# Kernel tuning notes

Measured on AMD Instinct MI355X. Metric: run time of the kernel, lower is better.

## Reference

```python
import jax, jax.numpy as jnp
import numpy as np

B, T_ENC, ENC_DIM = 32, 200, 256
T_DEC, DEC_OUT = 200, 80
HID = 256
PRENET1, PRENET2 = 256, 128


def _gru_cell(x, h, kernel, rec_kernel, bias):
    # Keras GRUCell, reset_after=True. bias: [2, 3*units] (input bias, recurrent bias)
    xz, xr, xh = jnp.split(x @ kernel + bias[0], 3, axis=-1)
    rz, rr, rh = jnp.split(h @ rec_kernel + bias[1], 3, axis=-1)
    z = jax.nn.sigmoid(xz + rz)
    r = jax.nn.sigmoid(xr + rr)
    hh = jnp.tanh(xh + r * rh)
    return z * h + (1.0 - z) * hh


def setup_inputs() -> dict:
    key = jax.random.key(0)
    ks = jax.random.split(key, 24)
    g = lambda k, shape: (jax.random.normal(k, shape, dtype=jnp.float32) / np.sqrt(shape[0] if len(shape) > 1 else 1.0))
    attn_in = PRENET2 + ENC_DIM  # prenet output concat prev attention
    return {
        "memory": jax.random.normal(ks[0], (B, T_ENC, ENC_DIM), dtype=jnp.float32),
        "dec_inputs": jax.random.normal(ks[1], (B, T_DEC, DEC_OUT), dtype=jnp.float32),
        # Prenet
        "fc1_w": g(ks[2], (DEC_OUT, PRENET1)), "fc1_b": jnp.zeros((PRENET1,), jnp.float32),
        "fc2_w": g(ks[3], (PRENET1, PRENET2)), "fc2_b": jnp.zeros((PRENET2,), jnp.float32),
        # Attention GRU cell
        "attn_k": g(ks[4], (attn_in, 3 * HID)), "attn_rk": g(ks[5], (HID, 3 * HID)),
        "attn_bias": jnp.zeros((2, 3 * HID), jnp.float32),
        # Bahdanau attention
        "W": g(ks[6], (ENC_DIM, ENC_DIM)), "U": g(ks[7], (HID, ENC_DIM)), "V": g(ks[8], (ENC_DIM, 1)),
        # Projection
        "proj_w": g(ks[9], (ENC_DIM + HID, HID)), "proj_b": jnp.zeros((HID,), jnp.float32),
        # Decoder GRU cells
        "rnn1_k": g(ks[10], (HID, 3 * HID)), "rnn1_rk": g(ks[11], (HID, 3 * HID)),
        "rnn1_bias": jnp.zeros((2, 3 * HID), jnp.float32),
        "rnn2_k": g(ks[12], (HID, 3 * HID)), "rnn2_rk": g(ks[13], (HID, 3 * HID)),
        "rnn2_bias": jnp.zeros((2, 3 * HID), jnp.float32),
        # Output projection
        "out_w": g(ks[14], (HID, DEC_OUT)), "out_b": jnp.zeros((DEC_OUT,), jnp.float32),
    }


def reference(memory, dec_inputs, fc1_w, fc1_b, fc2_w, fc2_b, attn_k, attn_rk,
              attn_bias, W, U, V, proj_w, proj_b, rnn1_k, rnn1_rk, rnn1_bias,
              rnn2_k, rnn2_rk, rnn2_bias, out_w, out_b):
    b = memory.shape[0]
    # W(values) is loop-invariant -> precompute (same math as in-step application)
    Wv = memory @ W  # [B, T_enc, ENC_DIM]

    def step(carry, x_t):
        attn, h_a, h1, h2 = carry
        # Prenet (Dropout is identity at inference)
        q = jax.nn.relu(x_t @ fc1_w + fc1_b)
        q = jax.nn.relu(q @ fc2_w + fc2_b)
        # Attention RNN
        h_a = _gru_cell(jnp.concatenate([q, attn], axis=-1), h_a, attn_k, attn_rk, attn_bias)
        # Bahdanau attention
        score = jnp.tanh(Wv + (h_a @ U)[:, None, :]) @ V           # [B, T_enc, 1]
        align = jax.nn.softmax(score, axis=1)                       # [B, T_enc, 1]
        attn = jnp.sum(align * memory, axis=1)                      # [B, ENC_DIM]
        # Projection + 2 decoder GRU cells with residual adds
        proj = jnp.concatenate([attn, h_a], axis=-1) @ proj_w + proj_b
        h1 = _gru_cell(proj, h1, rnn1_k, rnn1_rk, rnn1_bias)
        r1 = proj + h1
        h2 = _gru_cell(r1, h2, rnn2_k, rnn2_rk, rnn2_bias)
        r2 = r1 + h2
        out = r2 @ out_w + out_b
        return (attn, h_a, h1, h2), out

    init = (
        jnp.zeros((b, memory.shape[2]), memory.dtype),  # attention
        jnp.zeros((b, HID), memory.dtype),              # attn rnn state
        jnp.zeros((b, HID), memory.dtype),              # dec rnn1 state
        jnp.zeros((b, HID), memory.dtype),              # dec rnn2 state
    )
    xs = jnp.swapaxes(dec_inputs, 0, 1)  # [T_dec, B, DEC_OUT]
    _, ys = jax.lax.scan(step, init, xs)
    return jnp.swapaxes(ys, 0, 1)  # all_outputs: [B, T_dec, DEC_OUT]
```

## Files before the change

### kernel.cpp

```cpp
#include <hip/hip_runtime.h>
#include <math.h>


#define TENC 200
#define TDEC 200

typedef short bf16x8 __attribute__((ext_vector_type(8)));
typedef float f32x4  __attribute__((ext_vector_type(4)));

#define O_H1B 8192
#define O_H2B 24576
#define O_R1B 40960
#define O_AT  57344
#define O_NPQ 73728
#define O_ZPQ 98304
#define O_PJ  98432
#define ZERO_FLOATS 106624
#define O_HAS 106624
#define O_Q2  (O_HAS + 200*32*256)
#define O_WV  (O_Q2 + 200*32*128)
#define O_R2S (O_WV + 32*200*256)
#define O_IMG (O_R2S + 200*32*256)

#define IMGA_OFF  0u
#define IMGC1_OFF 1327104u
#define IMGC2_OFF 1859584u
#define IMGD_OFF  2924544u

__device__ __forceinline__ float sigm(float x)  { return 1.0f / (1.0f + __expf(-x)); }
__device__ __forceinline__ float ftanh(float x) { return 1.0f - 2.0f / (1.0f + __expf(2.0f * x)); }

__device__ __forceinline__ unsigned short f2bf(float f) {
  union { float f; unsigned u; } v; v.f = f;
  return (unsigned short)((v.u + 0x7FFFu + ((v.u >> 16) & 1u)) >> 16);
}
__device__ __forceinline__ float bf2f(unsigned short h) {
  union { unsigned u; float f; } v; v.u = ((unsigned)h) << 16; return v.f;
}

__device__ __forceinline__ void gst(float* p, float v) {
  __hip_atomic_store(p, v, __ATOMIC_RELAXED, __HIP_MEMORY_SCOPE_AGENT);
}
__device__ __forceinline__ float gld(const float* p) {
  return __hip_atomic_load(p, __ATOMIC_RELAXED, __HIP_MEMORY_SCOPE_AGENT);
}

__device__ __forceinline__ void pollwait(const unsigned* p, unsigned tgt, bool act) {
  for (;;) {
    bool ok = true;
    if (act) ok = (__hip_atomic_load(p, __ATOMIC_RELAXED, __HIP_MEMORY_SCOPE_AGENT) >= tgt);
    if (__syncthreads_and((int)ok)) break;
    __builtin_amdgcn_s_sleep(2);
  }
  asm volatile("" ::: "memory");
}
__device__ __forceinline__ void set_flag(unsigned* f, unsigned v) {
  asm volatile("" ::: "memory");
  __builtin_amdgcn_s_waitcnt(0);
  __syncthreads();
  if (threadIdx.x == 0) {
    __hip_atomic_store(f, v, __ATOMIC_RELAXED, __HIP_MEMORY_SCOPE_AGENT);
  }
}

__global__ __launch_bounds__(256) void k_prep(
    const float* __restrict__ aK, const float* __restrict__ aRK,
    const float* __restrict__ Wp,
    const float* __restrict__ K1, const float* __restrict__ RK1,
    const float* __restrict__ K2, const float* __restrict__ RK2,
    unsigned short* __restrict__ img)
{
  int e = blockIdx.x * 256 + threadIdx.x;
  int id = blockIdx.y;
  float w = 0.f; size_t oh = 0, ol = 0;
  if (id == 0) {
    if (e >= 32*32*648) return;
    int k = e % 648, n = (e / 648) & 31, blk = e / (648*32);
    int u = blk*8 + (n & 7), g = n >> 3;
    if (k < 384) {
      w = (g==0) ? aK[(size_t)k*768+u] : (g==1) ? aK[(size_t)k*768+256+u]
        : (g==2) ? aK[(size_t)k*768+512+u] : 0.f;
    } else if (k < 640) {
      int kk = k - 384;
      w = (g==0) ? aRK[(size_t)kk*768+u] : (g==1) ? aRK[(size_t)kk*768+256+u]
        : (g==3) ? aRK[(size_t)kk*768+512+u] : 0.f;
    }
    size_t base = IMGA_OFF + (size_t)blk*2*32*648;
    oh = base + (size_t)n*648 + k; ol = oh + 32*648;
  } else if (id == 1) {
    if (e >= 32*16*520) return;
    int k = e % 520, n = (e / 520) & 15, blk = e / (520*16);
    if (n < 8 && k < 512) w = Wp[(size_t)k*256 + blk*8 + n];
    size_t base = IMGC1_OFF + (size_t)blk*2*16*520;
    oh = base + (size_t)n*520 + k; ol = oh + 16*520;
  } else {
    if (e >= 32*32*520) return;
    int k = e % 520, n = (e / 520) & 31, blk = e / (520*32);
    int u = blk*8 + (n & 7), g = n >> 3;
    const float* Kx = (id == 2) ? K1 : K2;
    const float* Rx = (id == 2) ? RK1 : RK2;
    if (k < 256) {
      w = (g==0) ? Kx[(size_t)k*768+u] : (g==1) ? Kx[(size_t)k*768+256+u]
        : (g==2) ? Kx[(size_t)k*768+512+u] : 0.f;
    } else if (k < 512) {
      int kk = k - 256;
      w = (g==0) ? Rx[(size_t)kk*768+u] : (g==1) ? Rx[(size_t)kk*768+256+u]
        : (g==3) ? Rx[(size_t)kk*768+512+u] : 0.f;
    }
    size_t base = ((id == 2) ? IMGC2_OFF : IMGD_OFF) + (size_t)blk*2*32*520;
    oh = base + (size_t)n*520 + k; ol = oh + 32*520;
  }
  unsigned short hi = f2bf(w);
  unsigned short lo = f2bf(w - bf2f(hi));
  img[oh] = hi; img[ol] = lo;
}

__global__ __launch_bounds__(256, 1) void k_scan8(
    const float* __restrict__ memg,
    const float* __restrict__ aB, const float* __restrict__ Uw,
    const float* __restrict__ Vw, const float* __restrict__ pb,
    const float* __restrict__ B1v, const float* __restrict__ B2v,
    float* __restrict__ ws)
{
  const int tid = threadIdx.x, bid = blockIdx.x;
  const int lane = tid & 63, wv = tid >> 6;
  unsigned* fl = (unsigned*)ws;
  float* fH1B = ws + O_H1B;  float* fH2B = ws + O_H2B;  float* fR1B = ws + O_R1B;
  float* fAT  = ws + O_AT;   float* fNPq = ws + O_NPQ;  float* fZPq = ws + O_ZPQ;
  float* fPJ  = ws + O_PJ;   float* fHAS = ws + O_HAS;
  float* fQ2  = ws + O_Q2;   float* fWV  = ws + O_WV;   float* fR2S = ws + O_R2S;
  const unsigned short* img = (const unsigned short*)(ws + O_IMG);

  __shared__ __align__(16) char smem[140544];

  if (bid < 32) {
    const int j = bid;
    unsigned* myflag = fl + j * 32;
    unsigned short* sW = (unsigned short*)smem;
    unsigned short* sX = (unsigned short*)(smem + 82944);
    float* sOut = (float*)(smem + 124416);
    float* sHP  = (float*)(smem + 129024);
    float* sB   = (float*)(smem + 130048);
    {
      const uint4* src = (const uint4*)(img + IMGA_OFF + (size_t)j*2*32*648);
      uint4* dst = (uint4*)sW;
      for (int i = tid; i < 82944/16; i += 256) dst[i] = src[i];
      if (tid < 8) {
        int u = j*8 + tid;
        sB[tid]      = aB[u]       + aB[768 + u];
        sB[8 + tid]  = aB[256 + u] + aB[1024 + u];
        sB[16 + tid] = aB[512 + u];
        sB[24 + tid] = aB[1280 + u];
      }
    }
    __syncthreads();
    for (int t = 0; t < TDEC; ++t) {
      for (int i = tid; i < 4096; i += 256) {
        int b = i >> 7, k = i & 127;
        sX[b*648 + k] = f2bf(fQ2[((size_t)t*32 + b)*128 + k]);
      }
      pollwait(fl + (128 + (tid & 31))*32, (unsigned)t, (t > 0) && (tid < 32));
      float* at = fAT + (size_t)((t-1) & 1)*8192;
      for (int i = tid; i < 8192; i += 256) {
        int b = i >> 8, d = i & 255;
        float v = (t > 0) ? gld(at + b*256 + d) : 0.f;
        sX[b*648 + 128 + d] = f2bf(v);
      }
      for (int i = tid; i < 8192; i += 256) {
        int b = i >> 8, d = i & 255;
        float v = (t > 0) ? gld(fHAS + ((size_t)(t-1)*32 + b)*256 + d) : 0.f;
        sX[b*648 + 384 + d] = f2bf(v);
      }
      { int b = tid >> 3, ul = tid & 7;
        sHP[tid] = (t > 0) ? gld(fHAS + ((size_t)(t-1)*32 + b)*256 + j*8 + ul) : 0.f; }
      __syncthreads();
      {
        const int mt = wv >> 1, nt = wv & 1;
        f32x4 acc = {0.f, 0.f, 0.f, 0.f};
        const unsigned short* xr = sX + (size_t)(mt*16 + (lane&15))*648 + ((lane>>4)*8);
        const unsigned short* wh = sW + (size_t)(nt*16 + (lane&15))*648 + ((lane>>4)*8);
        const unsigned short* wl = wh + 32*648;
        for (int kt = 0; kt < 20; ++kt) {
          bf16x8 a  = *(const bf16x8*)(xr + kt*32);
          bf16x8 bh = *(const bf16x8*)(wh + kt*32);
          bf16x8 bl = *(const bf16x8*)(wl + kt*32);
          acc = __builtin_amdgcn_mfma_f32_16x16x32_bf16(a, bh, acc, 0, 0, 0);
          acc = __builtin_amdgcn_mfma_f32_16x16x32_bf16(a, bl, acc, 0, 0, 0);
        }
        int r0 = mt*16 + ((lane>>4)<<2), c = nt*16 + (lane&15);
        #pragma unroll
        for (int i2 = 0; i2 < 4; ++i2) sOut[(r0+i2)*36 + c] = acc[i2];
      }
      __syncthreads();
      { int b = tid >> 3, ul = tid & 7;
        float z = sigm(sOut[b*36 + ul] + sB[ul]);
        float r = sigm(sOut[b*36 + 8 + ul] + sB[8+ul]);
        float hh = ftanh(sOut[b*36 + 16 + ul] + sB[16+ul] + r*(sOut[b*36 + 24 + ul] + sB[24+ul]));
        float hn = z * sHP[tid] + (1.0f - z) * hh;
        gst(fHAS + ((size_t)t*32 + b)*256 + j*8 + ul, hn);
      }
      set_flag(myflag, (unsigned)(t + 1));
    }
  } else if (bid < 160) {
    const int idx = bid - 32, b = idx >> 2, q = idx & 3;
    unsigned* myflag = fl + (32 + b*3 + (q - 1)) * 32;
    float* sWV  = (float*)smem;
    float* sMem = (float*)(smem + 52000);
    float* sV   = (float*)(smem + 104000);
    float* sHA  = (float*)(smem + 105024);
    float* sUh  = (float*)(smem + 106048);
    float* sE   = (float*)(smem + 107072);
    float* sZ   = (float*)(smem + 107328);
    float* sCtx = (float*)(smem + 107392);
    float* sZs  = (float*)(smem + 108416);
    for (int i = tid; i < 50*256; i += 256) {
      int r = i >> 8, d = i & 255;
      sWV[r*260 + d]  = fWV[((size_t)b*200 + q*50 + r)*256 + d];
      sMem[r*260 + d] = memg[((size_t)b*200 + q*50 + r)*256 + d];
    }
    sV[tid] = Vw[tid];
    __syncthreads();
    for (int t = 0; t < TDEC; ++t) {
      pollwait(fl + (tid & 31)*32, (unsigned)(t + 1), tid < 32);
      sHA[tid] = gld(fHAS + ((size_t)t*32 + b)*256 + tid);
      __syncthreads();
      {
        float acc = 0.f;
        #pragma unroll 8
        for (int k = 0; k < 256; ++k) acc += sHA[k] * Uw[(size_t)k*256 + tid];
        sUh[tid] = acc; }
      __syncthreads();
      { int r = tid >> 2, qd = tid & 3;
        float part = 0.f;
        if (r < 50) {
          const float* wvp = sWV + r*260 + qd*64;
          const float* uh = sUh + qd*64;
          const float* vv = sV + qd*64;
          #pragma unroll 8
          for (int i2 = 0; i2 < 64; ++i2) part += vv[i2] * ftanh(wvp[i2] + uh[i2]);
        }
        part += __shfl_down(part, 2, 4);
        part += __shfl_down(part, 1, 4);
        if (r < 50 && qd == 0) sE[r] = __expf(part);
      }
      __syncthreads();
      if (tid < 64) {
        float e = (tid < 50) ? sE[tid] : 0.f;
        #pragma unroll
        for (int off = 32; off; off >>= 1) e += __shfl_xor(e, off, 64);
        if (tid == 0) sZ[0] = e;
      }
      __syncthreads();
      { float acc = 0.f;
        #pragma unroll 2
        for (int r = 0; r < 50; ++r) acc += sE[r] * sMem[r*260 + tid];
        if (q) gst(fNPq + ((size_t)b*3 + q - 1)*256 + tid, acc);
        else   sCtx[tid] = acc; }
      if (q) {
        if (tid == 0) gst(fZPq + b*3 + q - 1, sZ[0]);
        set_flag(myflag, (unsigned)(t + 1));
      } else {
        { const unsigned* p; unsigned tg; bool act;
          if (tid < 3)                    { p = fl + (32 + b*3 + tid)*32; tg = (unsigned)(t+1); act = true; }
          else if (tid >= 32 && tid < 64) { p = fl + (160 + tid - 32)*32; tg = (unsigned)(t-1); act = (t >= 2); }
          else                            { p = fl;                       tg = 0u;              act = false; }
          pollwait(p, tg, act);
        }
        if (tid < 3) sZs[tid] = gld(fZPq + b*3 + tid);
        __syncthreads();
        float Zi = 1.0f / (sZ[0] + sZs[0] + sZs[1] + sZs[2]);
        float av = (sCtx[tid] + gld(fNPq + (size_t)(b*3 + 0)*256 + tid)
                             + gld(fNPq + (size_t)(b*3 + 1)*256 + tid)
                             + gld(fNPq + (size_t)(b*3 + 2)*256 + tid)) * Zi;
        gst(fAT + (size_t)(t & 1)*8192 + b*256 + tid, av);
        set_flag(fl + (128 + b)*32, (unsigned)(t + 1));
      }
    }
  } else if (bid < 192) {
    const int j = bid - 160;
    unsigned* flagC1 = fl + (160 + j) * 32;
    unsigned* flagC2 = fl + (192 + j) * 32;
    unsigned short* sW1 = (unsigned short*)smem;
    unsigned short* sW2 = (unsigned short*)(smem + 33280);
    unsigned short* sX  = (unsigned short*)(smem + 99840);
    float* sOut = (float*)(smem + 133120);
    float* sPJ  = (float*)(smem + 137728);
    float* sH1p = (float*)(smem + 138752);
    float* sB   = (float*)(smem + 139776);
    {
      const uint4* s1 = (const uint4*)(img + IMGC1_OFF + (size_t)j*2*16*520);
      uint4* d1 = (uint4*)sW1;
      for (int i = tid; i < 33280/16; i += 256) d1[i] = s1[i];
      const uint4* s2 = (const uint4*)(img + IMGC2_OFF + (size_t)j*2*32*520);
      uint4* d2 = (uint4*)sW2;
      for (int i = tid; i < 66560/16; i += 256) d2[i] = s2[i];
      if (tid < 8) {
        int u = j*8 + tid;
        sB[tid]      = B1v[u]       + B1v[768 + u];
        sB[8 + tid]  = B1v[256 + u] + B1v[1024 + u];
        sB[16 + tid] = B1v[512 + u];
        sB[24 + tid] = B1v[1280 + u];
        sB[32 + tid] = pb[u];
      }
    }
    __syncthreads();
    for (int t = 0; t < TDEC; ++t) {
      {
        const unsigned* p; unsigned tg; bool act;
        if (tid < 32)      { p = fl + (128 + tid)*32;       tg = (unsigned)(t+1); act = true; }
        else if (tid < 64) { p = fl + (192 + tid - 32)*32;  tg = (unsigned)t;     act = (t > 0); }
        else if (tid < 96) { p = fl + (224 + tid - 64)*32;  tg = (unsigned)(t-1); act = (t >= 2); }
        else               { p = fl;                        tg = 0u;              act = false; }
        pollwait(p, tg, act);
      }
      float* at = fAT + (size_t)(t & 1)*8192;
      for (int i = tid; i < 8192; i += 256) {
        int b = i >> 8, d = i & 255;
        sX[b*520 + d] = f2bf(gld(at + b*256 + d));
      }
      for (int i = tid; i < 8192; i += 256) {
        int b = i >> 8, d = i & 255;
        sX[b*520 + 256 + d] = f2bf(gld(fHAS + ((size_t)t*32 + b)*256 + d));
      }
      __syncthreads();
      if (wv < 2) {
        const int mt = wv;
        f32x4 acc = {0.f, 0.f, 0.f, 0.f};
        const unsigned short* xr = sX + (size_t)(mt*16 + (lane&15))*520 + ((lane>>4)*8);
        const unsigned short* wh = sW1 + (size_t)(lane&15)*520 + ((lane>>4)*8);
        const unsigned short* wl = wh + 16*520;
        for (int kt = 0; kt < 16; ++kt) {
          bf16x8 a  = *(const bf16x8*)(xr + kt*32);
          bf16x8 bh = *(const bf16x8*)(wh + kt*32);
          bf16x8 bl = *(const bf16x8*)(wl + kt*32);
          acc = __builtin_amdgcn_mfma_f32_16x16x32_bf16(a, bh, acc, 0, 0, 0);
          acc = __builtin_amdgcn_mfma_f32_16x16x32_bf16(a, bl, acc, 0, 0, 0);
        }
        int r0 = mt*16 + ((lane>>4)<<2), c = lane & 15;
        #pragma unroll
        for (int i2 = 0; i2 < 4; ++i2) sOut[(r0+i2)*36 + c] = acc[i2];
      }
      __syncthreads();
      { int b = tid >> 3, ul = tid & 7;
        float pj = sOut[b*36 + ul] + sB[32 + ul];
        sPJ[tid] = pj;
        gst(fPJ + (size_t)b*256 + j*8 + ul, pj); }
      set_flag(flagC1, (unsigned)(t + 1));
      pollwait(fl + (160 + (tid & 31))*32, (unsigned)(t + 1), tid < 32);
      for (int i = tid; i < 8192; i += 256) {
        int b = i >> 8, d = i & 255;
        sX[b*520 + d] = f2bf(gld(fPJ + (size_t)b*256 + d));
      }
      for (int i = tid; i < 8192; i += 256) {
        int b = i >> 8, d = i & 255;
        sX[b*520 + 256 + d] = f2bf(gld(fH1B + (size_t)(t & 1)*8192 + (size_t)b*256 + d));
      }
      { int b = tid >> 3, ul = tid & 7;
        sH1p[tid] = gld(fH1B + (size_t)(t & 1)*8192 + (size_t)b*256 + j*8 + ul); }
      __syncthreads();
      {
        const int mt = wv >> 1, nt = wv & 1;
        f32x4 acc = {0.f, 0.f, 0.f, 0.f};
        const unsigned short* xr = sX + (size_t)(mt*16 + (lane&15))*520 + ((lane>>4)*8);
        const unsigned short* wh = sW2 + (size_t)(nt*16 + (lane&15))*520 + ((lane>>4)*8);
        const unsigned short* wl = wh + 32*520;
        for (int kt = 0; kt < 16; ++kt) {
          bf16x8 a  = *(const bf16x8*)(xr + kt*32);
          bf16x8 bh = *(const bf16x8*)(wh + kt*32);
          bf16x8 bl = *(const bf16x8*)(wl + kt*32);
          acc = __builtin_amdgcn_mfma_f32_16x16x32_bf16(a, bh, acc, 0, 0, 0);
          acc = __builtin_amdgcn_mfma_f32_16x16x32_bf16(a, bl, acc, 0, 0, 0);
        }
        int r0 = mt*16 + ((lane>>4)<<2), c = nt*16 + (lane&15);
        #pragma unroll
        for (int i2 = 0; i2 < 4; ++i2) sOut[(r0+i2)*36 + c] = acc[i2];
      }
      __syncthreads();
      { int b = tid >> 3, ul = tid & 7;
        float z = sigm(sOut[b*36 + ul] + sB[ul]);
        float r = sigm(sOut[b*36 + 8 + ul] + sB[8+ul]);
        float hh = ftanh(sOut[b*36 + 16 + ul] + sB[16+ul] + r*(sOut[b*36 + 24 + ul] + sB[24+ul]));
        float hn = z * sH1p[tid] + (1.0f - z) * hh;
        gst(fH1B + (size_t)((t+1) & 1)*8192 + (size_t)b*256 + j*8 + ul, hn);
        gst(fR1B + (size_t)(t & 1)*8192 + (size_t)b*256 + j*8 + ul, sPJ[tid] + hn);
      }
      set_flag(flagC2, (unsigned)(t + 1));
    }
  } else {
    const int j = bid - 192;
    unsigned* myflag = fl + (224 + j) * 32;
    unsigned short* sW = (unsigned short*)smem;
    unsigned short* sX = (unsigned short*)(smem + 66560);
    float* sOut = (float*)(smem + 99840);
    float* sR1f = (float*)(smem + 104448);
    float* sH2p = (float*)(smem + 105472);
    float* sB   = (float*)(smem + 106496);
    {
      const uint4* s2 = (const uint4*)(img + IMGD_OFF + (size_t)j*2*32*520);
      uint4* d2 = (uint4*)sW;
      for (int i = tid; i < 66560/16; i += 256) d2[i] = s2[i];
      if (tid < 8) {
        int u = j*8 + tid;
        sB[tid]      = B2v[u]       + B2v[768 + u];
        sB[8 + tid]  = B2v[256 + u] + B2v[1024 + u];
        sB[16 + tid] = B2v[512 + u];
        sB[24 + tid] = B2v[1280 + u];
      }
    }
    __syncthreads();
    for (int t = 0; t < TDEC; ++t) {
      { const unsigned* p; unsigned tg; bool act;
        if (tid < 32)      { p = fl + (192 + tid)*32;       tg = (unsigned)(t+1); act = true; }
        else if (tid < 64) { p = fl + (224 + tid - 32)*32;  tg = (unsigned)t;     act = (t > 0); }
        else               { p = fl;                        tg = 0u;              act = false; }
        pollwait(p, tg, act);
      }
      for (int i = tid; i < 8192; i += 256) {
        int b = i >> 8, d = i & 255;
        sX[b*520 + d] = f2bf(gld(fR1B + (size_t)(t & 1)*8192 + (size_t)b*256 + d));
      }
      for (int i = tid; i < 8192; i += 256) {
        int b = i >> 8, d = i & 255;
        sX[b*520 + 256 + d] = f2bf(gld(fH2B + (size_t)(t & 1)*8192 + (size_t)b*256 + d));
      }
      { int b = tid >> 3, ul = tid & 7;
        sR1f[tid] = gld(fR1B + (size_t)(t & 1)*8192 + (size_t)b*256 + j*8 + ul);
        sH2p[tid] = gld(fH2B + (size_t)(t & 1)*8192 + (size_t)b*256 + j*8 + ul); }
      __syncthreads();
      { const int mt = wv >> 1, nt = wv & 1;
        f32x4 acc = {0.f, 0.f, 0.f, 0.f};
        const unsigned short* xr = sX + (size_t)(mt*16 + (lane&15))*520 + ((lane>>4)*8);
        const unsigned short* wh = sW + (size_t)(nt*16 + (lane&15))*520 + ((lane>>4)*8);
        const unsigned short* wl = wh + 32*520;
        for (int kt = 0; kt < 16; ++kt) {
          bf16x8 a  = *(const bf16x8*)(xr + kt*32);
          bf16x8 bh = *(const bf16x8*)(wh + kt*32);
          bf16x8 bl = *(const bf16x8*)(wl + kt*32);
          acc = __builtin_amdgcn_mfma_f32_16x16x32_bf16(a, bh, acc, 0, 0, 0);
          acc = __builtin_amdgcn_mfma_f32_16x16x32_bf16(a, bl, acc, 0, 0, 0);
        }
        int r0 = mt*16 + ((lane>>4)<<2), c = nt*16 + (lane&15);
        #pragma unroll
        for (int i2 = 0; i2 < 4; ++i2) sOut[(r0+i2)*36 + c] = acc[i2];
      }
      __syncthreads();
      { int b = tid >> 3, ul = tid & 7;
        float z = sigm(sOut[b*36 + ul] + sB[ul]);
        float r = sigm(sOut[b*36 + 8 + ul] + sB[8+ul]);
        float hh = ftanh(sOut[b*36 + 16 + ul] + sB[16+ul] + r*(sOut[b*36 + 24 + ul] + sB[24+ul]));
        float hn = z * sH2p[tid] + (1.0f - z) * hh;
        gst(fH2B + (size_t)((t+1) & 1)*8192 + (size_t)b*256 + j*8 + ul, hn);
        fR2S[((size_t)t*32 + b)*256 + j*8 + ul] = sR1f[tid] + hn;
      }
      set_flag(myflag, (unsigned)(t + 1));
    }
  }
}

__global__ __launch_bounds__(256) void k_wv(
    const float* __restrict__ mem, const float* __restrict__ W, float* __restrict__ wv)
{
  const int tile = blockIdx.x, b = blockIdx.y;
  const int t0 = tile * 8, tid = threadIdx.x;
  __shared__ float rows[2048];
  for (int i = tid; i < 2048; i += 256) rows[i] = mem[((size_t)b*TENC + t0)*256 + i];
  __syncthreads();
  float acc[8] = {0,0,0,0,0,0,0,0};
  for (int k = 0; k < 256; ++k) {
    float w = W[(size_t)k*256 + tid];
    #pragma unroll
    for (int tt = 0; tt < 8; ++tt) acc[tt] += rows[tt*256 + k] * w;
  }
  #pragma unroll
  for (int tt = 0; tt < 8; ++tt) wv[((size_t)b*TENC + t0 + tt)*256 + tid] = acc[tt];
}

__global__ __launch_bounds__(256) void k_prenet(
    const float* __restrict__ x, const float* __restrict__ w1, const float* __restrict__ b1,
    const float* __restrict__ w2, const float* __restrict__ b2, float* __restrict__ q2)
{
  const int tile = blockIdx.x, b = blockIdx.y;
  const int t0 = tile * 4, tid = threadIdx.x;
  __shared__ float xr[320];
  __shared__ float q1[1024];
  for (int i = tid; i < 320; i += 256) {
    int tt = i / 80, k = i - tt*80;
    xr[i] = x[((size_t)b*TDEC + t0 + tt)*80 + k];
  }
  __syncthreads();
  {
    float a0 = 0.f, a1 = 0.f, a2 = 0.f, a3 = 0.f;
    for (int k = 0; k < 80; ++k) {
      float w = w1[(size_t)k*256 + tid];
      a0 += xr[k]*w; a1 += xr[80+k]*w; a2 += xr[160+k]*w; a3 += xr[240+k]*w;
    }
    float bb = b1[tid];
    q1[tid]       = fmaxf(a0 + bb, 0.f);
    q1[256 + tid] = fmaxf(a1 + bb, 0.f);
    q1[512 + tid] = fmaxf(a2 + bb, 0.f);
    q1[768 + tid] = fmaxf(a3 + bb, 0.f);
  }
  __syncthreads();
  {
    const int jj = tid & 127, tp = tid >> 7;
    float c0 = 0.f, c1 = 0.f;
    for (int k = 0; k < 256; ++k) {
      float w = w2[(size_t)k*128 + jj];
      c0 += q1[(2*tp)*256 + k] * w;
      c1 += q1[(2*tp + 1)*256 + k] * w;
    }
    float bb = b2[jj];
    q2[(((size_t)t0 + 2*tp)*32 + b)*128 + jj]     = fmaxf(c0 + bb, 0.f);
    q2[(((size_t)t0 + 2*tp + 1)*32 + b)*128 + jj] = fmaxf(c1 + bb, 0.f);
  }
}

__global__ __launch_bounds__(128) void k_out(
    const float* __restrict__ r2, const float* __restrict__ wo,
    const float* __restrict__ bo, float* __restrict__ out)
{
  const int tb = blockIdx.x;
  const int t = tb >> 5, b = tb & 31, tid = threadIdx.x;
  __shared__ float row[256];
  for (int i = tid; i < 256; i += 128) row[i] = r2[(size_t)tb*256 + i];
  __syncthreads();
  if (tid < 80) {
    float acc = bo[tid];
    #pragma unroll 4
    for (int k = 0; k < 256; ++k) acc += row[k] * wo[(size_t)k*80 + tid];
    out[((size_t)b*TDEC + t)*80 + tid] = acc;
  }
}

extern "C" void kernel_launch(void* const* d_in, const int* in_sizes, int n_in,
                              void* d_out, int out_size, void* d_ws, size_t ws_size,
                              hipStream_t stream)
{
  const float* mem = (const float*)d_in[0];
  const float* dec = (const float*)d_in[1];
  const float* w1  = (const float*)d_in[2];
  const float* b1  = (const float*)d_in[3];
  const float* w2  = (const float*)d_in[4];
  const float* b2  = (const float*)d_in[5];
  const float* aK  = (const float*)d_in[6];
  const float* aRK = (const float*)d_in[7];
  const float* aB  = (const float*)d_in[8];
  const float* W   = (const float*)d_in[9];
  const float* U   = (const float*)d_in[10];
  const float* V   = (const float*)d_in[11];
  const float* Wp  = (const float*)d_in[12];
  const float* pb  = (const float*)d_in[13];
  const float* K1  = (const float*)d_in[14];
  const float* RK1 = (const float*)d_in[15];
  const float* B1v = (const float*)d_in[16];
  const float* K2  = (const float*)d_in[17];
  const float* RK2 = (const float*)d_in[18];
  const float* B2v = (const float*)d_in[19];
  const float* Wo  = (const float*)d_in[20];
  const float* bo  = (const float*)d_in[21];
  float* ws  = (float*)d_ws;
  float* out = (float*)d_out;

  hipMemsetAsync(ws, 0, (size_t)ZERO_FLOATS * sizeof(float), stream);
  k_prep<<<dim3(2592, 4), 256, 0, stream>>>(aK, aRK, Wp, K1, RK1, K2, RK2,
                                            (unsigned short*)(ws + O_IMG));
  k_wv<<<dim3(25, 32), 256, 0, stream>>>(mem, W, ws + O_WV);
  k_prenet<<<dim3(50, 32), 256, 0, stream>>>(dec, w1, b1, w2, b2, ws + O_Q2);
  k_scan8<<<224, 256, 0, stream>>>(mem, aB, U, V, pb, B1v, B2v, ws);
  k_out<<<6400, 128, 0, stream>>>(ws + O_R2S, Wo, bo, out);
}
```

Baseline: 6.461 ms.

## Merge split-attention blocks into one block per batch and vectorize flag-guarded exchanges

Each batch's attention now runs in a single block instead of four blocks that exchanged partial context sums and normalizers through global memory. This removes one cross-block flag hop and the merge step in every decoder step, and the persistent grid shrinks from 224 to 128 blocks. To fit in shared memory, W·memory is stored in bf16 and memory rows are streamed from global each step. U is also pre-converted to bf16, and state exchanges use 64-bit atomic loads and stores plus shared-memory carry of the previous hidden state. The costs are lower precision in the attention scores, more serial work per attention block on the critical path, and heavier per-step global memory reads.

```diff
diff --git a/kernel.cpp b/kernel.cpp
--- a/kernel.cpp
+++ b/kernel.cpp
@@ -7,16 +7,16 @@
 
 typedef short bf16x8 __attribute__((ext_vector_type(8)));
 typedef float f32x4  __attribute__((ext_vector_type(4)));
+typedef float f32x2  __attribute__((ext_vector_type(2)));
+typedef unsigned short u16x2 __attribute__((ext_vector_type(2)));
 
 #define O_H1B 8192
 #define O_H2B 24576
 #define O_R1B 40960
 #define O_AT  57344
-#define O_NPQ 73728
-#define O_ZPQ 98304
-#define O_PJ  98432
-#define ZERO_FLOATS 106624
-#define O_HAS 106624
+#define O_PJ  73728
+#define ZERO_FLOATS 81920
+#define O_HAS 81920
 #define O_Q2  (O_HAS + 200*32*256)
 #define O_WV  (O_Q2 + 200*32*128)
 #define O_R2S (O_WV + 32*200*256)
@@ -26,6 +26,7 @@
 #define IMGC1_OFF 1327104u
 #define IMGC2_OFF 1859584u
 #define IMGD_OFF  2924544u
+#define IMGU_OFF  3989504u
 
 __device__ __forceinline__ float sigm(float x)  { return 1.0f / (1.0f + __expf(-x)); }
 __device__ __forceinline__ float ftanh(float x) { return 1.0f - 2.0f / (1.0f + __expf(2.0f * x)); }
@@ -38,11 +39,15 @@
   union { unsigned u; float f; } v; v.u = ((unsigned)h) << 16; return v.f;
 }
 
-__device__ __forceinline__ void gst(float* p, float v) {
-  __hip_atomic_store(p, v, __ATOMIC_RELAXED, __HIP_MEMORY_SCOPE_AGENT);
-}
-__device__ __forceinline__ float gld(const float* p) {
-  return __hip_atomic_load(p, __ATOMIC_RELAXED, __HIP_MEMORY_SCOPE_AGENT);
+__device__ __forceinline__ f32x2 gld2(const float* p) {
+  unsigned long long u = __hip_atomic_load((const unsigned long long*)p,
+                          __ATOMIC_RELAXED, __HIP_MEMORY_SCOPE_AGENT);
+  union { unsigned long long u; f32x2 f; } c; c.u = u; return c.f;
+}
+__device__ __forceinline__ void gst2(float* p, float a, float b) {
+  union { unsigned long long u; float f[2]; } c; c.f[0] = a; c.f[1] = b;
+  __hip_atomic_store((unsigned long long*)p, c.u,
+                     __ATOMIC_RELAXED, __HIP_MEMORY_SCOPE_AGENT);
 }
 
 __device__ __forceinline__ void pollwait(const unsigned* p, unsigned tgt, bool act) {
@@ -68,11 +73,16 @@
     const float* __restrict__ Wp,
     const float* __restrict__ K1, const float* __restrict__ RK1,
     const float* __restrict__ K2, const float* __restrict__ RK2,
+    const float* __restrict__ Uw,
     unsigned short* __restrict__ img)
 {
   int e = blockIdx.x * 256 + threadIdx.x;
   int id = blockIdx.y;
   float w = 0.f; size_t oh = 0, ol = 0;
+  if (id == 4) {
+    if (e < 256*256) img[IMGU_OFF + e] = f2bf(Uw[e]);
+    return;
+  }
   if (id == 0) {
     if (e >= 32*32*648) return;
     int k = e % 648, n = (e / 648) & 31, blk = e / (648*32);
@@ -115,10 +125,10 @@
   img[oh] = hi; img[ol] = lo;
 }
 
-__global__ __launch_bounds__(256, 1) void k_scan8(
+__global__ __launch_bounds__(256, 1) void k_scan9(
     const float* __restrict__ memg,
-    const float* __restrict__ aB, const float* __restrict__ Uw,
-    const float* __restrict__ Vw, const float* __restrict__ pb,
+    const float* __restrict__ aB, const float* __restrict__ Vw,
+    const float* __restrict__ pb,
     const float* __restrict__ B1v, const float* __restrict__ B2v,
     float* __restrict__ ws)
 {
@@ -126,8 +136,7 @@
   const int lane = tid & 63, wv = tid >> 6;
   unsigned* fl = (unsigned*)ws;
   float* fH1B = ws + O_H1B;  float* fH2B = ws + O_H2B;  float* fR1B = ws + O_R1B;
-  float* fAT  = ws + O_AT;   float* fNPq = ws + O_NPQ;  float* fZPq = ws + O_ZPQ;
-  float* fPJ  = ws + O_PJ;   float* fHAS = ws + O_HAS;
+  float* fAT  = ws + O_AT;   float* fPJ  = ws + O_PJ;   float* fHAS = ws + O_HAS;
   float* fQ2  = ws + O_Q2;   float* fWV  = ws + O_WV;   float* fR2S = ws + O_R2S;
   const unsigned short* img = (const unsigned short*)(ws + O_IMG);
 
@@ -139,7 +148,7 @@
     unsigned short* sW = (unsigned short*)smem;
     unsigned short* sX = (unsigned short*)(smem + 82944);
     float* sOut = (float*)(smem + 124416);
-    float* sHP  = (float*)(smem + 129024);
+    float* sHNp = (float*)(smem + 129024);
     float* sB   = (float*)(smem + 130048);
     {
       const uint4* src = (const uint4*)(img + IMGA_OFF + (size_t)j*2*32*648);
@@ -152,27 +161,29 @@
         sB[16 + tid] = aB[512 + u];
         sB[24 + tid] = aB[1280 + u];
       }
+      sHNp[tid & 255] = 0.f;
     }
     __syncthreads();
     for (int t = 0; t < TDEC; ++t) {
-      for (int i = tid; i < 4096; i += 256) {
-        int b = i >> 7, k = i & 127;
-        sX[b*648 + k] = f2bf(fQ2[((size_t)t*32 + b)*128 + k]);
-      }
-      pollwait(fl + (128 + (tid & 31))*32, (unsigned)t, (t > 0) && (tid < 32));
+      for (int i = tid; i < 2048; i += 256) {
+        int b = i >> 6, dp = i & 63;
+        f32x2 v = *(const f32x2*)(fQ2 + ((size_t)t*32 + b)*128 + dp*2);
+        *(u16x2*)(sX + b*648 + dp*2) = (u16x2){f2bf(v.x), f2bf(v.y)};
+      }
+      pollwait(fl + (32 + (tid & 31))*32, (unsigned)t, (t > 0) && (tid < 32));
       float* at = fAT + (size_t)((t-1) & 1)*8192;
-      for (int i = tid; i < 8192; i += 256) {
-        int b = i >> 8, d = i & 255;
-        float v = (t > 0) ? gld(at + b*256 + d) : 0.f;
-        sX[b*648 + 128 + d] = f2bf(v);
-      }
-      for (int i = tid; i < 8192; i += 256) {
-        int b = i >> 8, d = i & 255;
-        float v = (t > 0) ? gld(fHAS + ((size_t)(t-1)*32 + b)*256 + d) : 0.f;
-        sX[b*648 + 384 + d] = f2bf(v);
-      }
-      { int b = tid >> 3, ul = tid & 7;
-        sHP[tid] = (t > 0) ? gld(fHAS + ((size_t)(t-1)*32 + b)*256 + j*8 + ul) : 0.f; }
+      for (int i = tid; i < 4096; i += 256) {
+        int b = i >> 7, dp = i & 127;
+        f32x2 v; if (t > 0) v = gld2(at + b*256 + dp*2); else { v.x = 0.f; v.y = 0.f; }
+        *(u16x2*)(sX + b*648 + 128 + dp*2) = (u16x2){f2bf(v.x), f2bf(v.y)};
+      }
+      for (int i = tid; i < 4096; i += 256) {
+        int b = i >> 7, dp = i & 127;
+        f32x2 v;
+        if (t > 0) v = gld2(fHAS + ((size_t)(t-1)*32 + b)*256 + dp*2);
+        else { v.x = 0.f; v.y = 0.f; }
+        *(u16x2*)(sX + b*648 + 384 + dp*2) = (u16x2){f2bf(v.x), f2bf(v.y)};
+      }
       __syncthreads();
       {
         const int mt = wv >> 1, nt = wv & 1;
@@ -196,97 +207,93 @@
         float z = sigm(sOut[b*36 + ul] + sB[ul]);
         float r = sigm(sOut[b*36 + 8 + ul] + sB[8+ul]);
         float hh = ftanh(sOut[b*36 + 16 + ul] + sB[16+ul] + r*(sOut[b*36 + 24 + ul] + sB[24+ul]));
-        float hn = z * sHP[tid] + (1.0f - z) * hh;
-        gst(fHAS + ((size_t)t*32 + b)*256 + j*8 + ul, hn);
+        float hn = z * sHNp[tid] + (1.0f - z) * hh;
+        sHNp[tid] = hn;
+      }
+      __syncthreads();
+      if (tid < 128) { int b = tid >> 2, ulp = tid & 3;
+        gst2(fHAS + ((size_t)t*32 + b)*256 + j*8 + ulp*2,
+             sHNp[b*8 + ulp*2], sHNp[b*8 + ulp*2 + 1]);
       }
       set_flag(myflag, (unsigned)(t + 1));
     }
-  } else if (bid < 160) {
-    const int idx = bid - 32, b = idx >> 2, q = idx & 3;
-    unsigned* myflag = fl + (32 + b*3 + (q - 1)) * 32;
-    float* sWV  = (float*)smem;
-    float* sMem = (float*)(smem + 52000);
-    float* sV   = (float*)(smem + 104000);
-    float* sHA  = (float*)(smem + 105024);
-    float* sUh  = (float*)(smem + 106048);
-    float* sE   = (float*)(smem + 107072);
-    float* sZ   = (float*)(smem + 107328);
-    float* sCtx = (float*)(smem + 107392);
-    float* sZs  = (float*)(smem + 108416);
-    for (int i = tid; i < 50*256; i += 256) {
+  } else if (bid < 64) {
+    const int b = bid - 32;
+    unsigned* myflag = fl + (32 + b) * 32;
+    unsigned short* sWV = (unsigned short*)smem;
+    float* sV   = (float*)(smem + 105600);
+    float* sHA  = (float*)(smem + 106624);
+    float* sUh  = (float*)(smem + 107648);
+    float* sE   = (float*)(smem + 108672);
+    float* sCtx = (float*)(smem + 109504);
+    float* sRed = (float*)(smem + 110528);
+    const unsigned short* imgU = img + IMGU_OFF;
+    for (int i = tid; i < 200*256; i += 256) {
       int r = i >> 8, d = i & 255;
-      sWV[r*260 + d]  = fWV[((size_t)b*200 + q*50 + r)*256 + d];
-      sMem[r*260 + d] = memg[((size_t)b*200 + q*50 + r)*256 + d];
+      int qd = d >> 6, s = d & 63;
+      sWV[qd*13200 + r*66 + s] = f2bf(fWV[((size_t)b*200 + r)*256 + d]);
     }
     sV[tid] = Vw[tid];
     __syncthreads();
     for (int t = 0; t < TDEC; ++t) {
       pollwait(fl + (tid & 31)*32, (unsigned)(t + 1), tid < 32);
-      sHA[tid] = gld(fHAS + ((size_t)t*32 + b)*256 + tid);
+      if (tid < 128) {
+        f32x2 h = gld2(fHAS + ((size_t)t*32 + b)*256 + tid*2);
+        sHA[tid*2] = h.x; sHA[tid*2 + 1] = h.y;
+      }
       __syncthreads();
       {
         float acc = 0.f;
         #pragma unroll 8
-        for (int k = 0; k < 256; ++k) acc += sHA[k] * Uw[(size_t)k*256 + tid];
+        for (int k = 0; k < 256; ++k) acc += sHA[k] * bf2f(imgU[k*256 + tid]);
         sUh[tid] = acc; }
       __syncthreads();
-      { int r = tid >> 2, qd = tid & 3;
-        float part = 0.f;
-        if (r < 50) {
-          const float* wvp = sWV + r*260 + qd*64;
-          const float* uh = sUh + qd*64;
-          const float* vv = sV + qd*64;
-          #pragma unroll 8
-          for (int i2 = 0; i2 < 64; ++i2) part += vv[i2] * ftanh(wvp[i2] + uh[i2]);
+      { int rr = tid >> 2, qd = tid & 3;
+        const float* uh = sUh + qd*64;
+        const float* vv = sV + qd*64;
+        #pragma unroll
+        for (int p = 0; p < 4; ++p) {
+          int r = p*64 + rr;
+          bool on = (p < 3) || (rr < 8);
+          float part = 0.f;
+          if (on) {
+            const unsigned short* wvp = sWV + qd*13200 + r*66;
+            #pragma unroll 8
+            for (int i2 = 0; i2 < 64; ++i2) part += vv[i2] * ftanh(bf2f(wvp[i2]) + uh[i2]);
+          }
+          part += __shfl_down(part, 2, 4);
+          part += __shfl_down(part, 1, 4);
+          if (on && qd == 0) sE[r] = __expf(part);
         }
-        part += __shfl_down(part, 2, 4);
-        part += __shfl_down(part, 1, 4);
-        if (r < 50 && qd == 0) sE[r] = __expf(part);
-      }
-      __syncthreads();
-      if (tid < 64) {
-        float e = (tid < 50) ? sE[tid] : 0.f;
+      }
+      __syncthreads();
+      { float e = (tid < TENC) ? sE[tid] : 0.f;
         #pragma unroll
         for (int off = 32; off; off >>= 1) e += __shfl_xor(e, off, 64);
-        if (tid == 0) sZ[0] = e;
-      }
-      __syncthreads();
-      { float acc = 0.f;
-        #pragma unroll 2
-        for (int r = 0; r < 50; ++r) acc += sE[r] * sMem[r*260 + tid];
-        if (q) gst(fNPq + ((size_t)b*3 + q - 1)*256 + tid, acc);
-        else   sCtx[tid] = acc; }
-      if (q) {
-        if (tid == 0) gst(fZPq + b*3 + q - 1, sZ[0]);
-        set_flag(myflag, (unsigned)(t + 1));
-      } else {
-        { const unsigned* p; unsigned tg; bool act;
-          if (tid < 3)                    { p = fl + (32 + b*3 + tid)*32; tg = (unsigned)(t+1); act = true; }
-          else if (tid >= 32 && tid < 64) { p = fl + (160 + tid - 32)*32; tg = (unsigned)(t-1); act = (t >= 2); }
-          else                            { p = fl;                       tg = 0u;              act = false; }
-          pollwait(p, tg, act);
-        }
-        if (tid < 3) sZs[tid] = gld(fZPq + b*3 + tid);
-        __syncthreads();
-        float Zi = 1.0f / (sZ[0] + sZs[0] + sZs[1] + sZs[2]);
-        float av = (sCtx[tid] + gld(fNPq + (size_t)(b*3 + 0)*256 + tid)
-                             + gld(fNPq + (size_t)(b*3 + 1)*256 + tid)
-                             + gld(fNPq + (size_t)(b*3 + 2)*256 + tid)) * Zi;
-        gst(fAT + (size_t)(t & 1)*8192 + b*256 + tid, av);
-        set_flag(fl + (128 + b)*32, (unsigned)(t + 1));
-      }
-    }
-  } else if (bid < 192) {
-    const int j = bid - 160;
-    unsigned* flagC1 = fl + (160 + j) * 32;
-    unsigned* flagC2 = fl + (192 + j) * 32;
+        if ((tid & 63) == 0) sRed[tid >> 6] = e; }
+      __syncthreads();
+      { float Zi = 1.0f / (sRed[0] + sRed[1] + sRed[2] + sRed[3]);
+        const float* mb = memg + (size_t)b*TENC*256 + tid;
+        float acc = 0.f;
+        #pragma unroll 4
+        for (int r = 0; r < TENC; ++r) acc += sE[r] * mb[(size_t)r*256];
+        sCtx[tid] = acc * Zi; }
+      pollwait(fl + (64 + (tid & 31))*32, (unsigned)(t - 1), (t >= 2) && (tid < 32));
+      if (tid < 128)
+        gst2(fAT + (size_t)(t & 1)*8192 + b*256 + tid*2, sCtx[tid*2], sCtx[tid*2 + 1]);
+      set_flag(myflag, (unsigned)(t + 1));
+    }
+  } else if (bid < 96) {
+    const int j = bid - 64;
+    unsigned* flagC1 = fl + (64 + j) * 32;
+    unsigned* flagC2 = fl + (96 + j) * 32;
     unsigned short* sW1 = (unsigned short*)smem;
     unsigned short* sW2 = (unsigned short*)(smem + 33280);
     unsigned short* sX  = (unsigned short*)(smem + 99840);
     float* sOut = (float*)(smem + 133120);
     float* sPJ  = (float*)(smem + 137728);
-    float* sH1p = (float*)(smem + 138752);
-    float* sB   = (float*)(smem + 139776);
+    float* sB   = (float*)(smem + 138752);
+    float* sH1p = (float*)(smem + 138944);
     {
       const uint4* s1 = (const uint4*)(img + IMGC1_OFF + (size_t)j*2*16*520);
       uint4* d1 = (uint4*)sW1;
@@ -302,25 +309,28 @@
         sB[24 + tid] = B1v[1280 + u];
         sB[32 + tid] = pb[u];
       }
+      sH1p[tid & 255] = 0.f;
     }
     __syncthreads();
     for (int t = 0; t < TDEC; ++t) {
       {
         const unsigned* p; unsigned tg; bool act;
-        if (tid < 32)      { p = fl + (128 + tid)*32;       tg = (unsigned)(t+1); act = true; }
-        else if (tid < 64) { p = fl + (192 + tid - 32)*32;  tg = (unsigned)t;     act = (t > 0); }
-        else if (tid < 96) { p = fl + (224 + tid - 64)*32;  tg = (unsigned)(t-1); act = (t >= 2); }
+        if (tid < 32)      { p = fl + (32 + tid)*32;        tg = (unsigned)(t+1); act = true; }
+        else if (tid < 64) { p = fl + (96 + tid - 32)*32;   tg = (unsigned)t;     act = (t > 0); }
+        else if (tid < 96) { p = fl + (128 + tid - 64)*32;  tg = (unsigned)(t-1); act = (t >= 2); }
         else               { p = fl;                        tg = 0u;              act = false; }
         pollwait(p, tg, act);
       }
       float* at = fAT + (size_t)(t & 1)*8192;
-      for (int i = tid; i < 8192; i += 256) {
-        int b = i >> 8, d = i & 255;
-        sX[b*520 + d] = f2bf(gld(at + b*256 + d));
-      }
-      for (int i = tid; i < 8192; i += 256) {
-        int b = i >> 8, d = i & 255;
-        sX[b*520 + 256 + d] = f2bf(gld(fHAS + ((size_t)t*32 + b)*256 + d));
+      for (int i = tid; i < 4096; i += 256) {
+        int b = i >> 7, dp = i & 127;
+        f32x2 v = gld2(at + b*256 + dp*2);
+        *(u16x2*)(sX + b*520 + dp*2) = (u16x2){f2bf(v.x), f2bf(v.y)};
+      }
+      for (int i = tid; i < 4096; i += 256) {
+        int b = i >> 7, dp = i & 127;
+        f32x2 v = gld2(fHAS + ((size_t)t*32 + b)*256 + dp*2);
+        *(u16x2*)(sX + b*520 + 256 + dp*2) = (u16x2){f2bf(v.x), f2bf(v.y)};
       }
       __syncthreads();
       if (wv < 2) {
@@ -342,21 +352,23 @@
       }
       __syncthreads();
       { int b = tid >> 3, ul = tid & 7;
-        float pj = sOut[b*36 + ul] + sB[32 + ul];
-        sPJ[tid] = pj;
-        gst(fPJ + (size_t)b*256 + j*8 + ul, pj); }
+        sPJ[tid] = sOut[b*36 + ul] + sB[32 + ul]; }
+      __syncthreads();
+      if (tid < 128) { int b = tid >> 2, ulp = tid & 3;
+        gst2(fPJ + (size_t)b*256 + j*8 + ulp*2, sPJ[b*8 + ulp*2], sPJ[b*8 + ulp*2 + 1]);
+      }
       set_flag(flagC1, (unsigned)(t + 1));
-      pollwait(fl + (160 + (tid & 31))*32, (unsigned)(t + 1), tid < 32);
-      for (int i = tid; i < 8192; i += 256) {
-        int b = i >> 8, d = i & 255;
-        sX[b*520 + d] = f2bf(gld(fPJ + (size_t)b*256 + d));
-      }
-      for (int i = tid; i < 8192; i += 256) {
-        int b = i >> 8, d = i & 255;
-        sX[b*520 + 256 + d] = f2bf(gld(fH1B + (size_t)(t & 1)*8192 + (size_t)b*256 + d));
-      }
-      { int b = tid >> 3, ul = tid & 7;
-        sH1p[tid] = gld(fH1B + (size_t)(t & 1)*8192 + (size_t)b*256 + j*8 + ul); }
+      pollwait(fl + (64 + (tid & 31))*32, (unsigned)(t + 1), tid < 32);
+      for (int i = tid; i < 4096; i += 256) {
+        int b = i >> 7, dp = i & 127;
+        f32x2 v = gld2(fPJ + (size_t)b*256 + dp*2);
+        *(u16x2*)(sX + b*520 + dp*2) = (u16x2){f2bf(v.x), f2bf(v.y)};
+      }
+      for (int i = tid; i < 4096; i += 256) {
+        int b = i >> 7, dp = i & 127;
+        f32x2 v = gld2(fH1B + (size_t)(t & 1)*8192 + (size_t)b*256 + dp*2);
+        *(u16x2*)(sX + b*520 + 256 + dp*2) = (u16x2){f2bf(v.x), f2bf(v.y)};
+      }
       __syncthreads();
       {
         const int mt = wv >> 1, nt = wv & 1;
@@ -381,14 +393,23 @@
         float r = sigm(sOut[b*36 + 8 + ul] + sB[8+ul]);
         float hh = ftanh(sOut[b*36 + 16 + ul] + sB[16+ul] + r*(sOut[b*36 + 24 + ul] + sB[24+ul]));
         float hn = z * sH1p[tid] + (1.0f - z) * hh;
-        gst(fH1B + (size_t)((t+1) & 1)*8192 + (size_t)b*256 + j*8 + ul, hn);
-        gst(fR1B + (size_t)(t & 1)*8192 + (size_t)b*256 + j*8 + ul, sPJ[tid] + hn);
+        float r1 = sPJ[tid] + hn;
+        sH1p[tid] = hn;
+        __syncthreads();
+        sOut[tid] = hn; sOut[256 + tid] = r1;
+      }
+      __syncthreads();
+      if (tid < 128) { int b = tid >> 2, ulp = tid & 3;
+        gst2(fH1B + (size_t)((t+1) & 1)*8192 + (size_t)b*256 + j*8 + ulp*2,
+             sOut[b*8 + ulp*2], sOut[b*8 + ulp*2 + 1]);
+        gst2(fR1B + (size_t)(t & 1)*8192 + (size_t)b*256 + j*8 + ulp*2,
+             sOut[256 + b*8 + ulp*2], sOut[256 + b*8 + ulp*2 + 1]);
       }
       set_flag(flagC2, (unsigned)(t + 1));
     }
   } else {
-    const int j = bid - 192;
-    unsigned* myflag = fl + (224 + j) * 32;
+    const int j = bid - 96;
+    unsigned* myflag = fl + (128 + j) * 32;
     unsigned short* sW = (unsigned short*)smem;
     unsigned short* sX = (unsigned short*)(smem + 66560);
     float* sOut = (float*)(smem + 99840);
@@ -406,26 +427,29 @@
         sB[16 + tid] = B2v[512 + u];
         sB[24 + tid] = B2v[1280 + u];
       }
+      sH2p[tid & 255] = 0.f;
     }
     __syncthreads();
     for (int t = 0; t < TDEC; ++t) {
       { const unsigned* p; unsigned tg; bool act;
-        if (tid < 32)      { p = fl + (192 + tid)*32;       tg = (unsigned)(t+1); act = true; }
-        else if (tid < 64) { p = fl + (224 + tid - 32)*32;  tg = (unsigned)t;     act = (t > 0); }
+        if (tid < 32)      { p = fl + (96 + tid)*32;        tg = (unsigned)(t+1); act = true; }
+        else if (tid < 64) { p = fl + (128 + tid - 32)*32;  tg = (unsigned)t;     act = (t > 0); }
         else               { p = fl;                        tg = 0u;              act = false; }
         pollwait(p, tg, act);
       }
-      for (int i = tid; i < 8192; i += 256) {
-        int b = i >> 8, d = i & 255;
-        sX[b*520 + d] = f2bf(gld(fR1B + (size_t)(t & 1)*8192 + (size_t)b*256 + d));
-      }
-      for (int i = tid; i < 8192; i += 256) {
-        int b = i >> 8, d = i & 255;
-        sX[b*520 + 256 + d] = f2bf(gld(fH2B + (size_t)(t & 1)*8192 + (size_t)b*256 + d));
-      }
-      { int b = tid >> 3, ul = tid & 7;
-        sR1f[tid] = gld(fR1B + (size_t)(t & 1)*8192 + (size_t)b*256 + j*8 + ul);
-        sH2p[tid] = gld(fH2B + (size_t)(t & 1)*8192 + (size_t)b*256 + j*8 + ul); }
+      for (int i = tid; i < 4096; i += 256) {
+        int b = i >> 7, dp = i & 127;
+        f32x2 v = gld2(fR1B + (size_t)(t & 1)*8192 + (size_t)b*256 + dp*2);
+        *(u16x2*)(sX + b*520 + dp*2) = (u16x2){f2bf(v.x), f2bf(v.y)};
+        if ((dp*2 >> 3) == (unsigned)j) {
+          sR1f[b*8 + (dp*2 & 7)] = v.x; sR1f[b*8 + (dp*2 & 7) + 1] = v.y;
+        }
+      }
+      for (int i = tid; i < 4096; i += 256) {
+        int b = i >> 7, dp = i & 127;
+        f32x2 v = gld2(fH2B + (size_t)(t & 1)*8192 + (size_t)b*256 + dp*2);
+        *(u16x2*)(sX + b*520 + 256 + dp*2) = (u16x2){f2bf(v.x), f2bf(v.y)};
+      }
       __syncthreads();
       { const int mt = wv >> 1, nt = wv & 1;
         f32x4 acc = {0.f, 0.f, 0.f, 0.f};
@@ -449,8 +473,16 @@
         float r = sigm(sOut[b*36 + 8 + ul] + sB[8+ul]);
         float hh = ftanh(sOut[b*36 + 16 + ul] + sB[16+ul] + r*(sOut[b*36 + 24 + ul] + sB[24+ul]));
         float hn = z * sH2p[tid] + (1.0f - z) * hh;
-        gst(fH2B + (size_t)((t+1) & 1)*8192 + (size_t)b*256 + j*8 + ul, hn);
-        fR2S[((size_t)t*32 + b)*256 + j*8 + ul] = sR1f[tid] + hn;
+        float r2 = sR1f[tid] + hn;
+        sH2p[tid] = hn;
+        fR2S[((size_t)t*32 + b)*256 + j*8 + ul] = r2;
+        __syncthreads();
+        sOut[tid] = hn;
+      }
+      __syncthreads();
+      if (tid < 128) { int b = tid >> 2, ulp = tid & 3;
+        gst2(fH2B + (size_t)((t+1) & 1)*8192 + (size_t)b*256 + j*8 + ulp*2,
+             sOut[b*8 + ulp*2], sOut[b*8 + ulp*2 + 1]);
       }
       set_flag(myflag, (unsigned)(t + 1));
     }
@@ -562,10 +594,10 @@
   float* out = (float*)d_out;
 
   hipMemsetAsync(ws, 0, (size_t)ZERO_FLOATS * sizeof(float), stream);
-  k_prep<<<dim3(2592, 4), 256, 0, stream>>>(aK, aRK, Wp, K1, RK1, K2, RK2,
+  k_prep<<<dim3(2592, 5), 256, 0, stream>>>(aK, aRK, Wp, K1, RK1, K2, RK2, U,
                                             (unsigned short*)(ws + O_IMG));
   k_wv<<<dim3(25, 32), 256, 0, stream>>>(mem, W, ws + O_WV);
   k_prenet<<<dim3(50, 32), 256, 0, stream>>>(dec, w1, b1, w2, b2, ws + O_Q2);
-  k_scan8<<<224, 256, 0, stream>>>(mem, aB, U, V, pb, B1v, B2v, ws);
+  k_scan9<<<128, 256, 0, stream>>>(mem, aB, V, pb, B1v, B2v, ws);
   k_out<<<6400, 128, 0, stream>>>(ws + O_R2S, Wo, bo, out);
 }
```

New measurement: 7.322 ms. +13.3%, slower.
